# Kernel optimization log

Measured on AMD Instinct MI355X. Metric: run time of the kernel, lower is better.

Reference implementation:

```python
import jax, jax.numpy as jnp
import numpy as np

INPUT_DIM, QK_DIM, V_DIM = 1024, 512, 512

def setup_inputs() -> dict:
    key = jax.random.key(0)
    ks = jax.random.split(key, 7)
    B, S = 4, 2048
    scale = 1.0 / np.sqrt(INPUT_DIM)
    return {
        "x": jax.random.normal(ks[0], (B, S, INPUT_DIM), dtype=jnp.float32),
        "Wq": jax.random.normal(ks[1], (INPUT_DIM, QK_DIM), dtype=jnp.float32) * scale,
        "bq": jax.random.normal(ks[2], (QK_DIM,), dtype=jnp.float32) * 0.01,
        "Wk": jax.random.normal(ks[3], (INPUT_DIM, QK_DIM), dtype=jnp.float32) * scale,
        "bk": jax.random.normal(ks[4], (QK_DIM,), dtype=jnp.float32) * 0.01,
        "Wv": jax.random.normal(ks[5], (INPUT_DIM, V_DIM), dtype=jnp.float32) * scale,
        "bv": jax.random.normal(ks[6], (V_DIM,), dtype=jnp.float32) * 0.01,
    }

def reference(x, Wq, bq, Wk, bk, Wv, bv):
    # q,k: (B,S,Dqk), v: (B,S,Dv)
    q = jnp.einsum("bsi,id->bsd", x, Wq) + bq
    k = jnp.einsum("bsi,id->bsd", x, Wk) + bk
    v = jnp.einsum("bsi,id->bsd", x, Wv) + bv
    scale = 1.0 / jnp.sqrt(jnp.asarray(q.shape[-1], q.dtype))
    scores = jnp.einsum("bqd,bkd->bqk", q, k) * scale  # (B,S,S)
    attn = jax.nn.softmax(scores, axis=-1)
    return jnp.einsum("bqk,bkd->bqd", attn, v)
```

## Files before the change

kernel.cpp:

```cpp
#include <hip/hip_runtime.h>

typedef __attribute__((ext_vector_type(8))) short short8;
typedef __attribute__((ext_vector_type(4))) float f32x4;

#define S_    2048
#define DI    1024
#define DQK   512
#define DV    512
#define NTOK  8192
#define CSTR  136

#define GLL(gp, lp) __builtin_amdgcn_global_load_lds( \
    (const __attribute__((address_space(1))) unsigned int*)(gp), \
    (__attribute__((address_space(3))) unsigned int*)(lp), 16, 0, 0)

static __device__ __forceinline__ unsigned short f2bf(float f) {
  unsigned int u = __float_as_uint(f);
  u += 0x7fffu + ((u >> 16) & 1u);
  return (unsigned short)(u >> 16);
}

__global__ void prep_kernel(const float* __restrict__ x, unsigned short* __restrict__ xb,
                            const float* __restrict__ W0, const float* __restrict__ W1,
                            const float* __restrict__ W2,
                            unsigned short* __restrict__ T0, unsigned short* __restrict__ T1,
                            unsigned short* __restrict__ T2,
                            float* __restrict__ rowsum) {
  __shared__ float tile[32][33];
  int bid = blockIdx.x;
  if (bid < 4096) {
    int idx = (bid * 256 + threadIdx.x) * 8;
    const float4* p = (const float4*)(x + idx);
    float4 f0 = p[0], f1 = p[1];
    uint4 o;
    o.x = (unsigned)f2bf(f0.x) | ((unsigned)f2bf(f0.y) << 16);
    o.y = (unsigned)f2bf(f0.z) | ((unsigned)f2bf(f0.w) << 16);
    o.z = (unsigned)f2bf(f1.x) | ((unsigned)f2bf(f1.y) << 16);
    o.w = (unsigned)f2bf(f1.z) | ((unsigned)f2bf(f1.w) << 16);
    *(uint4*)(xb + idx) = o;
    return;
  }
  int b2 = bid - 4096;
  int mat = b2 >> 9;
  int rem = b2 & 511;
  if (mat == 0 && rem < 32) rowsum[rem * 256 + threadIdx.x] = 0.f;
  const float* W = (mat == 0) ? W0 : (mat == 1) ? W1 : W2;
  unsigned short* T = (mat == 0) ? T0 : (mat == 1) ? T1 : T2;
  int n0 = (rem & 15) * 32, k0 = (rem >> 4) * 32;
  int c = threadIdx.x & 31, r0 = threadIdx.x >> 5;
  for (int i = 0; i < 4; ++i) {
    int kk = r0 + i * 8;
    tile[kk][c] = W[(k0 + kk) * DQK + n0 + c];
  }
  __syncthreads();
  for (int i = 0; i < 4; ++i) {
    int nn = r0 + i * 8;
    T[(n0 + nn) * DI + k0 + c] = f2bf(tile[c][nn]);
  }
}

__device__ __forceinline__ void gemm_core_dbuf(
    const unsigned short* __restrict__ A, const unsigned short* __restrict__ B,
    int lda, int ldb, int K, int m0, int n0,
    unsigned short (*As)[128 * 32], unsigned short (*Bs)[128 * 32],
    f32x4 (&acc)[4][4]) {
  int tid = threadIdx.x, lane = tid & 63, wv = tid >> 6;
  int quad = lane >> 4, l16 = lane & 15;
  int wm = wv >> 1, wn = wv & 1;
  int srow = tid >> 2;
  int sc = (tid & 3) ^ (srow & 3);
  const unsigned short* gA0 = A + (size_t)(m0 + srow) * lda + sc * 8;
  const unsigned short* gA1 = A + (size_t)(m0 + 64 + srow) * lda + sc * 8;
  const unsigned short* gB0 = B + (size_t)(n0 + srow) * ldb + sc * 8;
  const unsigned short* gB1 = B + (size_t)(n0 + 64 + srow) * ldb + sc * 8;
  int d0 = wv * 512;
  int d1 = 2048 + wv * 512;
#pragma unroll
  for (int i = 0; i < 4; ++i)
#pragma unroll
    for (int j = 0; j < 4; ++j) acc[i][j] = (f32x4){0.f, 0.f, 0.f, 0.f};

  auto stage = [&](int buf, int k0) {
    GLL(gA0 + k0, &As[buf][d0]);
    GLL(gA1 + k0, &As[buf][d1]);
    GLL(gB0 + k0, &Bs[buf][d0]);
    GLL(gB1 + k0, &Bs[buf][d1]);
  };

  int pc = (quad ^ (l16 & 3)) * 8;
  int nk = K >> 5;
  stage(0, 0);
  for (int kt = 0; kt < nk; ++kt) {
    int cur = kt & 1;
    __syncthreads();
    if (kt + 1 < nk) stage(cur ^ 1, (kt + 1) * 32);
    short8 af[4], bf[4];
#pragma unroll
    for (int t = 0; t < 4; ++t) {
      af[t] = *(const short8*)(&As[cur][(wm * 64 + t * 16 + l16) * 32 + pc]);
      bf[t] = *(const short8*)(&Bs[cur][(wn * 64 + t * 16 + l16) * 32 + pc]);
    }
#pragma unroll
    for (int tm = 0; tm < 4; ++tm)
#pragma unroll
      for (int tn = 0; tn < 4; ++tn)
        acc[tm][tn] = __builtin_amdgcn_mfma_f32_16x16x32_bf16(af[tm], bf[tn], acc[tm][tn], 0, 0, 0);
  }
}

__global__ __launch_bounds__(256, 3) void qkv_dma_kernel(
    const unsigned short* __restrict__ xb,
    const unsigned short* __restrict__ wqt, const unsigned short* __restrict__ wkt,
    const unsigned short* __restrict__ wvt,
    const float* __restrict__ bq, const float* __restrict__ bk, const float* __restrict__ bv,
    unsigned short* __restrict__ qo, unsigned short* __restrict__ ko,
    unsigned short* __restrict__ vto) {
  __shared__ unsigned short smem[128 * CSTR];
  unsigned short (*As)[4096] = (unsigned short (*)[4096])smem;
  unsigned short (*Bs)[4096] = (unsigned short (*)[4096])(smem + 8192);
  int bidx = blockIdx.x;
  int xcd = bidx & 7;
  int local = bidx >> 3;
  int mlocal = local & 7;
  int col12 = local >> 3;
  int mat = col12 >> 2;
  int m0 = (xcd * 8 + mlocal) * 128;
  int n0 = (col12 & 3) * 128;
  const unsigned short* wt = (mat == 0) ? wqt : (mat == 1) ? wkt : wvt;
  const float* bias = (mat == 0) ? bq : (mat == 1) ? bk : bv;
  float oscale = (mat == 0) ? 0.04419417382415922f : 1.0f;
  f32x4 acc[4][4];
  gemm_core_dbuf(xb, wt, DI, DI, DI, m0, n0, As, Bs, acc);

  int tid = threadIdx.x, lane = tid & 63, wv = tid >> 6;
  int quad = lane >> 4, l16 = lane & 15;
  int wm = wv >> 1, wn = wv & 1;
  bool transp = (mat == 2);
  __syncthreads();
#pragma unroll
  for (int tn = 0; tn < 4; ++tn) {
    int cl = wn * 64 + tn * 16 + l16;
    float bc = bias[n0 + cl];
#pragma unroll
    for (int tm = 0; tm < 4; ++tm) {
      int rl = wm * 64 + tm * 16 + quad * 4;
      f32x4 a = acc[tm][tn];
      unsigned short v0 = f2bf((a.x + bc) * oscale);
      unsigned short v1 = f2bf((a.y + bc) * oscale);
      unsigned short v2 = f2bf((a.z + bc) * oscale);
      unsigned short v3 = f2bf((a.w + bc) * oscale);
      if (!transp) {
        smem[(rl + 0) * CSTR + cl] = v0;
        smem[(rl + 1) * CSTR + cl] = v1;
        smem[(rl + 2) * CSTR + cl] = v2;
        smem[(rl + 3) * CSTR + cl] = v3;
      } else {
        smem[cl * CSTR + rl + 0] = v0;
        smem[cl * CSTR + rl + 1] = v1;
        smem[cl * CSTR + rl + 2] = v2;
        smem[cl * CSTR + rl + 3] = v3;
      }
    }
  }
  __syncthreads();
  int r = tid >> 1, half = (tid & 1) * 64;
  if (!transp) {
    unsigned short* outp = (mat == 0) ? qo : ko;
    unsigned short* gp = outp + (size_t)(m0 + r) * DQK + n0 + half;
#pragma unroll
    for (int j = 0; j < 8; ++j)
      *(uint4*)(gp + j * 8) = *(const uint4*)(smem + r * CSTR + half + j * 8);
  } else {
    unsigned short* gp = vto + (size_t)(n0 + r) * NTOK + m0 + half;
#pragma unroll
    for (int j = 0; j < 8; ++j)
      *(uint4*)(gp + j * 8) = *(const uint4*)(smem + r * CSTR + half + j * 8);
  }
}

__global__ __launch_bounds__(256, 4) void s_exp_kernel(
    const unsigned short* __restrict__ q, const unsigned short* __restrict__ k,
    unsigned short* __restrict__ sp, float* __restrict__ rowsum) {
  __shared__ unsigned short smem[128 * CSTR];
  unsigned short (*As)[4096] = (unsigned short (*)[4096])smem;
  unsigned short (*Bs)[4096] = (unsigned short (*)[4096])(smem + 8192);
  int bidx = blockIdx.x;
  int xcd = bidx & 7, b = xcd >> 1;
  int sub = ((bidx >> 3) << 1) | (xcd & 1);
  int m0 = (sub >> 4) * 128, n0 = (sub & 15) * 128;
  f32x4 acc[4][4];
  gemm_core_dbuf(q + (size_t)b * S_ * DQK, k + (size_t)b * S_ * DQK,
                 DQK, DQK, DQK, m0, n0, As, Bs, acc);

  int tid = threadIdx.x, lane = tid & 63, wv = tid >> 6;
  int quad = lane >> 4, l16 = lane & 15;
  int wm = wv >> 1, wn = wv & 1;
  __syncthreads();
#pragma unroll
  for (int tm = 0; tm < 4; ++tm) {
    int rl = wm * 64 + tm * 16 + quad * 4;
    float rs[4] = {0.f, 0.f, 0.f, 0.f};
#pragma unroll
    for (int tn = 0; tn < 4; ++tn) {
      int cl = wn * 64 + tn * 16 + l16;
      f32x4 a = acc[tm][tn];
      float e0 = __expf(a.x), e1 = __expf(a.y), e2 = __expf(a.z), e3 = __expf(a.w);
      smem[(rl + 0) * CSTR + cl] = f2bf(e0);
      smem[(rl + 1) * CSTR + cl] = f2bf(e1);
      smem[(rl + 2) * CSTR + cl] = f2bf(e2);
      smem[(rl + 3) * CSTR + cl] = f2bf(e3);
      rs[0] += e0; rs[1] += e1; rs[2] += e2; rs[3] += e3;
    }
    for (int off = 1; off < 16; off <<= 1)
#pragma unroll
      for (int r = 0; r < 4; ++r) rs[r] += __shfl_xor(rs[r], off);
    if (l16 == 0)
#pragma unroll
      for (int r = 0; r < 4; ++r) atomicAdd(rowsum + b * S_ + m0 + rl + r, rs[r]);
  }
  __syncthreads();
  int r = tid >> 1, half = (tid & 1) * 64;
  unsigned short* gp = sp + (size_t)b * S_ * S_ + (size_t)(m0 + r) * S_ + n0 + half;
#pragma unroll
  for (int j = 0; j < 8; ++j)
    *(uint4*)(gp + j * 8) = *(const uint4*)(smem + r * CSTR + half + j * 8);
}

__global__ __launch_bounds__(256, 4) void pv_kernel(
    const unsigned short* __restrict__ sp, const unsigned short* __restrict__ vt,
    const float* __restrict__ rowsum, float* __restrict__ out) {
  __shared__ unsigned short smem[16384];
  unsigned short (*As)[4096] = (unsigned short (*)[4096])smem;
  unsigned short (*Bs)[4096] = (unsigned short (*)[4096])(smem + 8192);
  int bidx = blockIdx.x;
  int xcd = bidx & 7, b = xcd >> 1;
  int sub = ((bidx >> 3) << 1) | (xcd & 1);
  int m0 = (sub >> 3) * 64, n0 = (sub & 7) * 64;
  int tid = threadIdx.x, lane = tid & 63, wv = tid >> 6;
  int quad = lane >> 4, l16 = lane & 15;
  int wm = wv >> 1, wn = wv & 1;
  const unsigned short* A = sp + (size_t)b * S_ * S_;
  const unsigned short* B = vt + (size_t)b * S_;

  int srow = tid >> 3;
  int schunk = (tid & 7) ^ (srow & 7);
  const unsigned short* gA0 = A + (size_t)(m0 + srow) * S_ + schunk * 8;
  const unsigned short* gA1 = A + (size_t)(m0 + 32 + srow) * S_ + schunk * 8;
  const unsigned short* gB0 = B + (size_t)(n0 + srow) * NTOK + schunk * 8;
  const unsigned short* gB1 = B + (size_t)(n0 + 32 + srow) * NTOK + schunk * 8;
  int ldsw0 = (wv * 8) * 64;
  int ldsw1 = (32 + wv * 8) * 64;

  f32x4 acc[2][2];
#pragma unroll
  for (int i = 0; i < 2; ++i)
#pragma unroll
    for (int j = 0; j < 2; ++j) acc[i][j] = (f32x4){0.f, 0.f, 0.f, 0.f};

  auto stage = [&](int buf, int k0) {
    GLL(gA0 + k0, &As[buf][ldsw0]);
    GLL(gA1 + k0, &As[buf][ldsw1]);
    GLL(gB0 + k0, &Bs[buf][ldsw0]);
    GLL(gB1 + k0, &Bs[buf][ldsw1]);
  };

  stage(0, 0);
  for (int kt = 0; kt < 32; ++kt) {
    int cur = kt & 1;
    __syncthreads();
    if (kt + 1 < 32) stage(cur ^ 1, (kt + 1) * 64);
#pragma unroll
    for (int ks = 0; ks < 2; ++ks) {
      int pc = ((ks * 4 + quad) ^ (l16 & 7)) * 8;
      short8 af[2], bf[2];
#pragma unroll
      for (int t = 0; t < 2; ++t) {
        af[t] = *(const short8*)(&As[cur][(wm * 32 + t * 16 + l16) * 64 + pc]);
        bf[t] = *(const short8*)(&Bs[cur][(wn * 32 + t * 16 + l16) * 64 + pc]);
      }
#pragma unroll
      for (int tm = 0; tm < 2; ++tm)
#pragma unroll
        for (int tn = 0; tn < 2; ++tn)
          acc[tm][tn] = __builtin_amdgcn_mfma_f32_16x16x32_bf16(af[tm], bf[tn], acc[tm][tn], 0, 0, 0);
    }
  }

  float* ct = (float*)smem;
  __syncthreads();
#pragma unroll
  for (int tm = 0; tm < 2; ++tm) {
    int rl = wm * 32 + tm * 16 + quad * 4;
    float inv[4];
#pragma unroll
    for (int i = 0; i < 4; ++i) inv[i] = 1.0f / rowsum[b * S_ + m0 + rl + i];
#pragma unroll
    for (int tn = 0; tn < 2; ++tn) {
      int cl = wn * 32 + tn * 16 + l16;
      f32x4 a = acc[tm][tn];
      ct[(rl + 0) * 68 + cl] = a.x * inv[0];
      ct[(rl + 1) * 68 + cl] = a.y * inv[1];
      ct[(rl + 2) * 68 + cl] = a.z * inv[2];
      ct[(rl + 3) * 68 + cl] = a.w * inv[3];
    }
  }
  __syncthreads();
  int r = tid >> 2, qc = (tid & 3) * 16;
  float* ob = out + (size_t)b * S_ * DV + (size_t)(m0 + r) * DV + n0 + qc;
#pragma unroll
  for (int j = 0; j < 4; ++j)
    *(uint4*)(ob + j * 4) = *(const uint4*)(ct + r * 68 + qc + j * 4);
}

extern "C" void kernel_launch(void* const* d_in, const int* in_sizes, int n_in,
                              void* d_out, int out_size, void* d_ws, size_t ws_size,
                              hipStream_t stream) {
  const float* x  = (const float*)d_in[0];
  const float* Wq = (const float*)d_in[1];
  const float* bq = (const float*)d_in[2];
  const float* Wk = (const float*)d_in[3];
  const float* bk = (const float*)d_in[4];
  const float* Wv = (const float*)d_in[5];
  const float* bv = (const float*)d_in[6];
  float* out = (float*)d_out;

  char* ws = (char*)d_ws;
  unsigned short* xb  = (unsigned short*)(ws);
  unsigned short* wqt = (unsigned short*)(ws + 16777216);
  unsigned short* wkt = (unsigned short*)(ws + 16777216 + 1048576);
  unsigned short* wvt = (unsigned short*)(ws + 16777216 + 2097152);
  unsigned short* qo  = (unsigned short*)(ws + 19922944);
  unsigned short* ko  = (unsigned short*)(ws + 19922944 + 8388608);
  unsigned short* vto = (unsigned short*)(ws + 19922944 + 16777216);
  unsigned short* sp  = (unsigned short*)(ws + 45088768);
  float* rowsum       = (float*)(ws + 45088768 + 33554432);

  prep_kernel<<<5632, 256, 0, stream>>>(x, xb, Wq, Wk, Wv, wqt, wkt, wvt, rowsum);
  qkv_dma_kernel<<<768, 256, 0, stream>>>(xb, wqt, wkt, wvt, bq, bk, bv, qo, ko, vto);
  s_exp_kernel<<<1024, 256, 0, stream>>>(qo, ko, sp, rowsum);
  pv_kernel<<<1024, 256, 0, stream>>>(sp, vto, rowsum, out);
}
```

Baseline: 188.3 us.

## Enlarge score-exp tile to 128x256 with inline double-buffered MFMA loop

The QK^T + exp kernel now computes a 128x256 output tile per block instead of 128x128, using its own double-buffered global_load_lds pipeline with XOR swizzle rather than the shared gemm core. Exponentials are applied in registers, and the bf16 tile is written out in two 64-row halves through a wider shared staging buffer. This doubles reuse of the Q tile and halves the number of blocks and rowsum atomics. The cost is lower occupancy (launch bounds 2) and more accumulator registers.

```diff
diff --git a/kernel.cpp b/kernel.cpp
--- a/kernel.cpp
+++ b/kernel.cpp
@@ -9,6 +9,7 @@
 #define DV    512
 #define NTOK  8192
 #define CSTR  136
+#define CS2   264
 
 #define GLL(gp, lp) __builtin_amdgcn_global_load_lds( \
     (const __attribute__((address_space(1))) unsigned int*)(gp), \
@@ -178,38 +179,78 @@
   }
 }
 
-__global__ __launch_bounds__(256, 4) void s_exp_kernel(
+__global__ __launch_bounds__(256, 2) void s_exp_kernel(
     const unsigned short* __restrict__ q, const unsigned short* __restrict__ k,
     unsigned short* __restrict__ sp, float* __restrict__ rowsum) {
-  __shared__ unsigned short smem[128 * CSTR];
-  unsigned short (*As)[4096] = (unsigned short (*)[4096])smem;
-  unsigned short (*Bs)[4096] = (unsigned short (*)[4096])(smem + 8192);
+  __shared__ unsigned short smem[24576];
   int bidx = blockIdx.x;
   int xcd = bidx & 7, b = xcd >> 1;
   int sub = ((bidx >> 3) << 1) | (xcd & 1);
-  int m0 = (sub >> 4) * 128, n0 = (sub & 15) * 128;
-  f32x4 acc[4][4];
-  gemm_core_dbuf(q + (size_t)b * S_ * DQK, k + (size_t)b * S_ * DQK,
-                 DQK, DQK, DQK, m0, n0, As, Bs, acc);
-
+  int m0 = (sub >> 3) * 128, n0 = (sub & 7) * 256;
   int tid = threadIdx.x, lane = tid & 63, wv = tid >> 6;
   int quad = lane >> 4, l16 = lane & 15;
   int wm = wv >> 1, wn = wv & 1;
-  __syncthreads();
+  const unsigned short* qb = q + (size_t)b * S_ * DQK;
+  const unsigned short* kb = k + (size_t)b * S_ * DQK;
+
+  int srow = tid >> 2;
+  int sc = (tid & 3) ^ (srow & 3);
+  const unsigned short* gA0 = qb + (size_t)(m0 + srow) * DQK + sc * 8;
+  const unsigned short* gA1 = qb + (size_t)(m0 + 64 + srow) * DQK + sc * 8;
+  const unsigned short* gB0 = kb + (size_t)(n0 + srow) * DQK + sc * 8;
+  const unsigned short* gB1 = kb + (size_t)(n0 + 64 + srow) * DQK + sc * 8;
+  const unsigned short* gB2 = kb + (size_t)(n0 + 128 + srow) * DQK + sc * 8;
+  const unsigned short* gB3 = kb + (size_t)(n0 + 192 + srow) * DQK + sc * 8;
+  int dA0 = (wv * 16) * 32, dA1 = (64 + wv * 16) * 32;
+
+  f32x4 acc[4][8];
+#pragma unroll
+  for (int i = 0; i < 4; ++i)
+#pragma unroll
+    for (int j = 0; j < 8; ++j) acc[i][j] = (f32x4){0.f, 0.f, 0.f, 0.f};
+
+  auto stage = [&](int buf, int k0) {
+    unsigned short* base = smem + buf * 12288;
+    GLL(gA0 + k0, base + dA0);
+    GLL(gA1 + k0, base + dA1);
+    unsigned short* bb = base + 4096;
+    GLL(gB0 + k0, bb + dA0);
+    GLL(gB1 + k0, bb + dA1);
+    GLL(gB2 + k0, bb + (128 + wv * 16) * 32);
+    GLL(gB3 + k0, bb + (192 + wv * 16) * 32);
+  };
+
+  int pc = (quad ^ (l16 & 3)) * 8;
+  stage(0, 0);
+  for (int kt = 0; kt < 16; ++kt) {
+    int cur = kt & 1;
+    __syncthreads();
+    if (kt + 1 < 16) stage(cur ^ 1, (kt + 1) * 32);
+    const unsigned short* base = smem + cur * 12288;
+    short8 af[4], bf[8];
+#pragma unroll
+    for (int t = 0; t < 4; ++t)
+      af[t] = *(const short8*)(base + (wm * 64 + t * 16 + l16) * 32 + pc);
+#pragma unroll
+    for (int t = 0; t < 8; ++t)
+      bf[t] = *(const short8*)(base + 4096 + (wn * 128 + t * 16 + l16) * 32 + pc);
+#pragma unroll
+    for (int tm = 0; tm < 4; ++tm)
+#pragma unroll
+      for (int tn = 0; tn < 8; ++tn)
+        acc[tm][tn] = __builtin_amdgcn_mfma_f32_16x16x32_bf16(af[tm], bf[tn], acc[tm][tn], 0, 0, 0);
+  }
+
 #pragma unroll
   for (int tm = 0; tm < 4; ++tm) {
     int rl = wm * 64 + tm * 16 + quad * 4;
     float rs[4] = {0.f, 0.f, 0.f, 0.f};
 #pragma unroll
-    for (int tn = 0; tn < 4; ++tn) {
-      int cl = wn * 64 + tn * 16 + l16;
+    for (int tn = 0; tn < 8; ++tn) {
       f32x4 a = acc[tm][tn];
-      float e0 = __expf(a.x), e1 = __expf(a.y), e2 = __expf(a.z), e3 = __expf(a.w);
-      smem[(rl + 0) * CSTR + cl] = f2bf(e0);
-      smem[(rl + 1) * CSTR + cl] = f2bf(e1);
-      smem[(rl + 2) * CSTR + cl] = f2bf(e2);
-      smem[(rl + 3) * CSTR + cl] = f2bf(e3);
-      rs[0] += e0; rs[1] += e1; rs[2] += e2; rs[3] += e3;
+      a.x = __expf(a.x); a.y = __expf(a.y); a.z = __expf(a.z); a.w = __expf(a.w);
+      acc[tm][tn] = a;
+      rs[0] += a.x; rs[1] += a.y; rs[2] += a.z; rs[3] += a.w;
     }
     for (int off = 1; off < 16; off <<= 1)
 #pragma unroll
@@ -218,12 +259,33 @@
 #pragma unroll
       for (int r = 0; r < 4; ++r) atomicAdd(rowsum + b * S_ + m0 + rl + r, rs[r]);
   }
-  __syncthreads();
-  int r = tid >> 1, half = (tid & 1) * 64;
-  unsigned short* gp = sp + (size_t)b * S_ * S_ + (size_t)(m0 + r) * S_ + n0 + half;
-#pragma unroll
-  for (int j = 0; j < 8; ++j)
-    *(uint4*)(gp + j * 8) = *(const uint4*)(smem + r * CSTR + half + j * 8);
+
+  unsigned short* spb = sp + (size_t)b * S_ * S_;
+  int cr = tid >> 2, cq = (tid & 3) * 64;
+#pragma unroll
+  for (int h = 0; h < 2; ++h) {
+    __syncthreads();
+    if (wm == h) {
+#pragma unroll
+      for (int tm = 0; tm < 4; ++tm) {
+        int rl = tm * 16 + quad * 4;
+#pragma unroll
+        for (int tn = 0; tn < 8; ++tn) {
+          int cl = wn * 128 + tn * 16 + l16;
+          f32x4 a = acc[tm][tn];
+          smem[(rl + 0) * CS2 + cl] = f2bf(a.x);
+          smem[(rl + 1) * CS2 + cl] = f2bf(a.y);
+          smem[(rl + 2) * CS2 + cl] = f2bf(a.z);
+          smem[(rl + 3) * CS2 + cl] = f2bf(a.w);
+        }
+      }
+    }
+    __syncthreads();
+    unsigned short* gp = spb + (size_t)(m0 + h * 64 + cr) * S_ + n0 + cq;
+#pragma unroll
+    for (int j = 0; j < 8; ++j)
+      *(uint4*)(gp + j * 8) = *(const uint4*)(smem + cr * CS2 + cq + j * 8);
+  }
 }
 
 __global__ __launch_bounds__(256, 4) void pv_kernel(
@@ -337,6 +399,6 @@
 
   prep_kernel<<<5632, 256, 0, stream>>>(x, xb, Wq, Wk, Wv, wqt, wkt, wvt, rowsum);
   qkv_dma_kernel<<<768, 256, 0, stream>>>(xb, wqt, wkt, wvt, bq, bk, bv, qo, ko, vto);
-  s_exp_kernel<<<1024, 256, 0, stream>>>(qo, ko, sp, rowsum);
+  s_exp_kernel<<<512, 256, 0, stream>>>(qo, ko, sp, rowsum);
   pv_kernel<<<1024, 256, 0, stream>>>(sp, vto, rowsum, out);
 }
```

Result: no change. 186.1 us (-1.2%).
